# Kernel optimization log

Measured on AMD Instinct MI355X. Metric: run time of the kernel, lower is better.

The kernel has to match this reference:

```python
import jax, jax.numpy as jnp
import numpy as np

B, N, C = 2, 2048, 768
H, HD = 12, 64
HID = 3072
LN_EPS = 1e-5
POL_EPS = 1e-6


def _layer_norm(x, g, b):
    m = jnp.mean(x, axis=-1, keepdims=True)
    v = jnp.mean(jnp.square(x - m), axis=-1, keepdims=True)
    return (x - m) * jax.lax.rsqrt(v + LN_EPS) * g + b


def _softmax_with_policy(attn, policy):
    # attn: [B,H,N,N], policy: [B,N,1]
    n = attn.shape[-1]
    ap = policy.reshape(policy.shape[0], 1, 1, n)  # [B,1,1,N]
    eye = jnp.eye(n, dtype=ap.dtype)[None, None]   # [1,1,N,N]
    ap = ap + (1.0 - ap) * eye                     # always attend to self
    attn = attn - jnp.max(attn, axis=-1, keepdims=True)
    attn = jnp.exp(attn.astype(jnp.float32)) * ap.astype(jnp.float32)
    attn = (attn + POL_EPS / n) / (jnp.sum(attn, axis=-1, keepdims=True) + POL_EPS)
    return attn


def setup_inputs() -> dict:
    key = jax.random.key(0)
    ks = jax.random.split(key, 12)
    s = lambda fan_in: 1.0 / np.sqrt(fan_in)
    x = jax.random.normal(ks[0], (B, N, C), dtype=jnp.float32)
    policy = (jax.random.uniform(ks[1], (B, N, 1)) > 0.5).astype(jnp.float32)
    return {
        "x": x,
        "policy": policy,
        "ln1_g": jnp.ones((C,), jnp.float32),
        "ln1_b": jnp.zeros((C,), jnp.float32),
        "qkv_w": jax.random.uniform(ks[2], (3 * H * HD, C), jnp.float32, -s(C), s(C)),
        "proj_w": jax.random.uniform(ks[3], (C, H * HD), jnp.float32, -s(H * HD), s(H * HD)),
        "proj_b": jnp.zeros((C,), jnp.float32),
        "ln2_g": jnp.ones((C,), jnp.float32),
        "ln2_b": jnp.zeros((C,), jnp.float32),
        "fc1_w": jax.random.uniform(ks[4], (HID, C), jnp.float32, -s(C), s(C)),
        "fc1_b": jnp.zeros((HID,), jnp.float32),
        "fc2_w": jax.random.uniform(ks[5], (C, HID), jnp.float32, -s(HID), s(HID)),
        "fc2_b": jnp.zeros((C,), jnp.float32),
    }


def reference(x, policy, ln1_g, ln1_b, qkv_w, proj_w, proj_b, ln2_g, ln2_b, fc1_w, fc1_b, fc2_w, fc2_b):
    b, n, c = x.shape
    scale = HD ** -0.5
    # --- attention branch (pre-LN) ---
    h = _layer_norm(x, ln1_g, ln1_b)
    qkv = (h @ qkv_w.T).reshape(b, n, 3, H, HD).transpose(2, 0, 3, 1, 4)  # [3,B,H,N,hd]
    q, k, v = qkv[0], qkv[1], qkv[2]
    attn = jnp.einsum("bhqd,bhkd->bhqk", q * scale, k)
    attn = _softmax_with_policy(attn, policy).astype(x.dtype)
    o = jnp.einsum("bhqk,bhkd->bhqd", attn, v).transpose(0, 2, 1, 3).reshape(b, n, H * HD)
    x = x + (o @ proj_w.T + proj_b)  # skip_lam = 1.0, dropout/drop_path = identity
    # --- MLP branch (pre-LN) ---
    h = _layer_norm(x, ln2_g, ln2_b)
    h = jax.nn.gelu(h @ fc1_w.T + fc1_b, approximate=False)  # torch nn.GELU = exact erf
    x = x + (h @ fc2_w.T + fc2_b)
    return x
```

## Files before the change

kernel.cpp:

```cpp
#include <hip/hip_runtime.h>

typedef unsigned short u16;
typedef unsigned int u32;
typedef float f32x4 __attribute__((ext_vector_type(4)));
typedef float f32x16 __attribute__((ext_vector_type(16)));
typedef __bf16 bf16x8 __attribute__((ext_vector_type(8)));
typedef u16 u16x4v __attribute__((ext_vector_type(4)));
typedef u32 u32x2 __attribute__((ext_vector_type(2)));
typedef u32 u32x4 __attribute__((ext_vector_type(4)));

#define NHEAD 12
#define NN 2048
#define CC 768

#define GLOBAL_AS __attribute__((address_space(1)))
#define LDS_AS __attribute__((address_space(3)))

__device__ __forceinline__ u16 tobf(float f) {
  __bf16 h = (__bf16)f;
  return __builtin_bit_cast(u16, h);
}
__device__ __forceinline__ float bf2f(u16 h) {
  u32 u = ((u32)h) << 16;
  return __builtin_bit_cast(float, u);
}
__device__ __forceinline__ void plswap(u32& a, u32& b) {
  asm volatile("v_permlane32_swap_b32 %0, %1" : "+v"(a), "+v"(b));
}
__device__ __forceinline__ void plswapf(float& a, float& b) {
  asm volatile("v_permlane32_swap_b32 %0, %1" : "+v"(a), "+v"(b));
}

#define N4_QKV 442368
#define N4_PROJ 147456
#define N4_FC 589824
__global__ __launch_bounds__(256) void cvt4_kernel(
    const float* __restrict__ a, const float* __restrict__ b,
    const float* __restrict__ c, const float* __restrict__ d,
    u16* __restrict__ oa, u16* __restrict__ ob, u16* __restrict__ oc,
    u16* __restrict__ od) {
  int i = blockIdx.x * 256 + threadIdx.x;
  const float* src;
  u16* dst;
  if (i < N4_QKV) {
    src = a; dst = oa;
  } else if (i < N4_QKV + N4_PROJ) {
    i -= N4_QKV; src = b; dst = ob;
  } else if (i < N4_QKV + N4_PROJ + N4_FC) {
    i -= N4_QKV + N4_PROJ; src = c; dst = oc;
  } else {
    i -= N4_QKV + N4_PROJ + N4_FC; src = d; dst = od;
    if (i >= N4_FC) return;
  }
  float4 v = ((const float4*)src)[i];
  u16x4v o = {tobf(v.x), tobf(v.y), tobf(v.z), tobf(v.w)};
  ((u16x4v*)dst)[i] = o;
}

__global__ __launch_bounds__(256) void ln_kernel(const float* __restrict__ x,
                                                 const float* __restrict__ gw,
                                                 const float* __restrict__ bw,
                                                 u16* __restrict__ out) {
  int row = blockIdx.x * 4 + (threadIdx.x >> 6);
  int lane = threadIdx.x & 63;
  const float* xr = x + (size_t)row * CC + lane * 12;
  float v[12];
  *(float4*)&v[0] = *(const float4*)(xr + 0);
  *(float4*)&v[4] = *(const float4*)(xr + 4);
  *(float4*)&v[8] = *(const float4*)(xr + 8);
  float s = 0.f, sq = 0.f;
#pragma unroll
  for (int j = 0; j < 12; ++j) { s += v[j]; sq += v[j] * v[j]; }
#pragma unroll
  for (int o = 1; o < 64; o <<= 1) { s += __shfl_xor(s, o); sq += __shfl_xor(sq, o); }
  float mean = s * (1.f / CC);
  float var = sq * (1.f / CC) - mean * mean;
  float rs = rsqrtf(var + 1e-5f);
  u16 ob[12];
#pragma unroll
  for (int j = 0; j < 12; ++j) {
    int c = lane * 12 + j;
    ob[j] = tobf((v[j] - mean) * rs * gw[c] + bw[c]);
  }
  u32* orow = (u32*)(out + (size_t)row * CC + lane * 12);
#pragma unroll
  for (int j = 0; j < 6; ++j) orow[j] = (u32)ob[2 * j] | ((u32)ob[2 * j + 1] << 16);
}

template <int BM, int OB, int HASB, int ACT, int RES>
__global__ __launch_bounds__(256) void gemm_kernel(
    const u16* __restrict__ A, const u16* __restrict__ Bw,
    const float* __restrict__ bias, const float* __restrict__ res,
    void* __restrict__ Cout, int M, int N, int K) {
  constexpr int MW = BM / 2;
  constexpr int MF = MW / 16;
  __shared__ __align__(16) u16 Alds[BM * 64];
  __shared__ __align__(16) u16 Blds[128 * 64];
  const int tid = threadIdx.x;
  const int lane = tid & 63, wave = tid >> 6;
  const int l15 = lane & 15, g = lane >> 4;
  const int bm = blockIdx.x * BM, bn = blockIdx.y * 128;
  const int wm = (wave >> 1) * MW, wn = (wave & 1) * 64;
  f32x4 acc[MF][4] = {};

  for (int kt = 0; kt < K; kt += 64) {
#pragma unroll
    for (int i = 0; i < BM / 32; ++i) {
      int ob_ = i * 4096 + wave * 1024;
      int lb = ob_ + lane * 16;
      int row = lb >> 7;
      int cb = (lb & 127) ^ ((row & 7) << 4);
      const u16* sa = A + (size_t)(bm + row) * K + kt + (cb >> 1);
      __builtin_amdgcn_global_load_lds((const GLOBAL_AS void*)sa,
                                       (LDS_AS void*)(Alds + (ob_ >> 1)), 16, 0, 0);
    }
#pragma unroll
    for (int i = 0; i < 4; ++i) {
      int ob_ = i * 4096 + wave * 1024;
      int lb = ob_ + lane * 16;
      int row = lb >> 7;
      int cb = (lb & 127) ^ ((row & 7) << 4);
      const u16* sb = Bw + (size_t)(bn + row) * K + kt + (cb >> 1);
      __builtin_amdgcn_global_load_lds((const GLOBAL_AS void*)sb,
                                       (LDS_AS void*)(Blds + (ob_ >> 1)), 16, 0, 0);
    }
    __syncthreads();
#pragma unroll
    for (int ks = 0; ks < 2; ++ks) {
      bf16x8 af[MF], bfr[4];
#pragma unroll
      for (int mi = 0; mi < MF; ++mi) {
        int row = wm + mi * 16 + l15;
        int cb = (ks * 64 + g * 16) ^ ((row & 7) << 4);
        af[mi] = *(const bf16x8*)&Alds[row * 64 + (cb >> 1)];
      }
#pragma unroll
      for (int ni = 0; ni < 4; ++ni) {
        int row = wn + ni * 16 + l15;
        int cb = (ks * 64 + g * 16) ^ ((row & 7) << 4);
        bfr[ni] = *(const bf16x8*)&Blds[row * 64 + (cb >> 1)];
      }
#pragma unroll
      for (int mi = 0; mi < MF; ++mi)
#pragma unroll
        for (int ni = 0; ni < 4; ++ni)
          acc[mi][ni] = __builtin_amdgcn_mfma_f32_16x16x32_bf16(af[mi], bfr[ni],
                                                                acc[mi][ni], 0, 0, 0);
    }
    __syncthreads();
  }
#pragma unroll
  for (int mi = 0; mi < MF; ++mi) {
#pragma unroll
    for (int ni = 0; ni < 4; ++ni) {
      int col = bn + wn + ni * 16 + l15;
      float bs = HASB ? bias[col] : 0.f;
#pragma unroll
      for (int r = 0; r < 4; ++r) {
        int rowm = bm + wm + mi * 16 + g * 4 + r;
        float v = acc[mi][ni][r] + bs;
        if (ACT) v = 0.5f * v * (1.f + erff(v * 0.70710678118654752f));
        if (RES) v += res[(size_t)rowm * N + col];
        if (OB)
          ((u16*)Cout)[(size_t)rowm * N + col] = tobf(v);
        else
          ((float*)Cout)[(size_t)rowm * N + col] = v;
      }
    }
  }
}

__global__ __launch_bounds__(256) void vsum_kernel(const u16* __restrict__ qkv,
                                                   float* __restrict__ vs) {
  int bh = blockIdx.x, q4 = blockIdx.y;
  int b = bh / NHEAD, h = bh % NHEAD;
  int d = threadIdx.x & 63, part = threadIdx.x >> 6;
  float s = 0.f;
  for (int n = q4 * 512 + part; n < q4 * 512 + 512; n += 4)
    s += bf2f(qkv[(size_t)(b * NN + n) * 2304 + 2 * CC + h * 64 + d]);
  __shared__ float red[256];
  red[threadIdx.x] = s;
  __syncthreads();
  if (threadIdx.x < 64) {
    float t = red[threadIdx.x] + red[threadIdx.x + 64] + red[threadIdx.x + 128] +
              red[threadIdx.x + 192];
    vs[q4 * (24 * 64) + bh * 64 + threadIdx.x] = t;
  }
}

#define SCL2E 0.18033688f
#define TRRD(dst, addr, OFF) \
  asm volatile("ds_read_b64_tr_b16 %0, %1 offset:" OFF : "=v"(dst) : "v"(addr))

__global__ __launch_bounds__(256) void attn32_kernel(const u16* __restrict__ qkv,
                                                     const float* __restrict__ policy,
                                                     float* __restrict__ partO,
                                                     float* __restrict__ partlm) {
  __shared__ __align__(16) u16 Klds[2][4096];
  __shared__ __align__(16) u16 Vlds[2][4096];
  __shared__ u16 PolB[NN];
  __shared__ float alf[4][32];
  const int bh = blockIdx.y, b = bh / NHEAD, h = bh % NHEAD;
  const int qt = blockIdx.x >> 1, half = blockIdx.x & 1;
  const int tid = threadIdx.x, lane = tid & 63, w = tid >> 6;
  const int l31 = lane & 31, hp = lane >> 5, b4 = (lane >> 4) & 1;
  const int q0 = qt * 128 + w * 32;
  const int dv = q0 >> 6;
  const int ktd = (q0 >> 5) & 1;
  const int kv0 = half * 1024;
  const size_t adv = (size_t)64 * 2304;

  bf16x8 qf0, qf1, qf2, qf3;
  {
    const u16* qp = qkv + (size_t)(b * NN + q0 + l31) * 2304 + h * 64 + 8 * hp;
#pragma unroll
    for (int ds = 0; ds < 4; ++ds) {
      bf16x8 r = *(const bf16x8*)(qp + ds * 16);
      bf16x8 o;
#pragma unroll
      for (int j = 0; j < 8; ++j) o[j] = (__bf16)((float)r[j] * SCL2E);
      if (ds == 0) qf0 = o; else if (ds == 1) qf1 = o; else if (ds == 2) qf2 = o; else qf3 = o;
    }
  }

  const u16* ksrc[2];
  const u16* vsrcp[2];
#pragma unroll
  for (int c = 0; c < 2; ++c) {
    int lb = c * 4096 + w * 1024 + lane * 16;
    int row = lb >> 7;
    int cb = (lb & 127) ^ ((row & 7) << 4);
    ksrc[c] = qkv + (size_t)(b * NN + kv0 + row) * 2304 + CC + h * 64 + (cb >> 1);
    int idx0 = (c * 256 + w * 64 + lane) * 8;
    int s0 = idx0 & 15, jj = (idx0 >> 4) & 3, b4v = (idx0 >> 6) & 1,
        pv = (idx0 >> 7) & 1, hv = (idx0 >> 8) & 1, dtv = (idx0 >> 9) & 1,
        mkv = (idx0 >> 10) & 3;
    int key = mkv * 16 + 8 * hv + 4 * pv + jj;
    int d0 = dtv * 32 + 16 * b4v + s0;
    vsrcp[c] = qkv + (size_t)(b * NN + kv0 + key) * 2304 + 2 * CC + h * 64 + d0;
  }
  auto stage = [&](int buf) {
#pragma unroll
    for (int c = 0; c < 2; ++c) {
      __builtin_amdgcn_global_load_lds((const GLOBAL_AS void*)ksrc[c],
                                       (LDS_AS void*)&Klds[buf][c * 2048 + w * 512], 16, 0, 0);
      __builtin_amdgcn_global_load_lds((const GLOBAL_AS void*)vsrcp[c],
                                       (LDS_AS void*)&Vlds[buf][c * 2048 + w * 512], 16, 0, 0);
      ksrc[c] += adv; vsrcp[c] += adv;
    }
  };

  stage(0);
  {
    float4 p0 = *(const float4*)&policy[b * NN + tid * 8];
    float4 p1 = *(const float4*)&policy[b * NN + tid * 8 + 4];
    u16x4v a = {tobf(p0.x), tobf(p0.y), tobf(p0.z), tobf(p0.w)};
    u16x4v c2 = {tobf(p1.x), tobf(p1.y), tobf(p1.z), tobf(p1.w)};
    *(u16x4v*)&PolB[tid * 8] = a;
    *(u16x4v*)&PolB[tid * 8 + 4] = c2;
  }
  __syncthreads();

  float m_cur = -3.0e38f, m_true = -3.0e38f, l_run = 0.f;
  f32x16 accd[2] = {};
  const u32 vbase = (u32)(uintptr_t)(LDS_AS u16*)&Vlds[0][0] +
                    (u32)(2 * (lane & 15) + 128 * b4 + 512 * hp);

  for (int t = 0; t < 16; ++t) {
    const int cur = t & 1;
    const int kvg = kv0 + t * 64;
    if (t < 15) stage(cur ^ 1);

    f32x16 sv0, sv1;
    {
      bf16x8 kf[4];
#pragma unroll
      for (int ds = 0; ds < 4; ++ds) {
        int row = l31;
        int cb = (32 * ds + 16 * hp) ^ ((row & 7) << 4);
        kf[ds] = *(const bf16x8*)((const char*)&Klds[cur][0] + row * 128 + cb);
      }
      f32x16 a = {};
      a = __builtin_amdgcn_mfma_f32_32x32x16_bf16(kf[0], qf0, a, 0, 0, 0);
      a = __builtin_amdgcn_mfma_f32_32x32x16_bf16(kf[1], qf1, a, 0, 0, 0);
      a = __builtin_amdgcn_mfma_f32_32x32x16_bf16(kf[2], qf2, a, 0, 0, 0);
      a = __builtin_amdgcn_mfma_f32_32x32x16_bf16(kf[3], qf3, a, 0, 0, 0);
      sv0 = a;
    }
    {
      bf16x8 kf[4];
#pragma unroll
      for (int ds = 0; ds < 4; ++ds) {
        int row = 32 + l31;
        int cb = (32 * ds + 16 * hp) ^ ((row & 7) << 4);
        kf[ds] = *(const bf16x8*)((const char*)&Klds[cur][0] + row * 128 + cb);
      }
      f32x16 a = {};
      a = __builtin_amdgcn_mfma_f32_32x32x16_bf16(kf[0], qf0, a, 0, 0, 0);
      a = __builtin_amdgcn_mfma_f32_32x32x16_bf16(kf[1], qf1, a, 0, 0, 0);
      a = __builtin_amdgcn_mfma_f32_32x32x16_bf16(kf[2], qf2, a, 0, 0, 0);
      a = __builtin_amdgcn_mfma_f32_32x32x16_bf16(kf[3], qf3, a, 0, 0, 0);
      sv1 = a;
    }

    u32x2 tr[4][2][2];
    {
      u32 vab = vbase + (u32)(cur * 8192);
      TRRD(tr[0][0][0], vab, "0");    TRRD(tr[0][0][1], vab, "256");
      TRRD(tr[0][1][0], vab, "1024"); TRRD(tr[0][1][1], vab, "1280");
      TRRD(tr[1][0][0], vab, "2048"); TRRD(tr[1][0][1], vab, "2304");
      TRRD(tr[1][1][0], vab, "3072"); TRRD(tr[1][1][1], vab, "3328");
      TRRD(tr[2][0][0], vab, "4096"); TRRD(tr[2][0][1], vab, "4352");
      TRRD(tr[3][0][0], vab, "6144"); TRRD(tr[3][0][1], vab, "6400");
      TRRD(tr[2][1][0], vab, "5120"); TRRD(tr[2][1][1], vab, "5376");
      TRRD(tr[3][1][0], vab, "7168"); TRRD(tr[3][1][1], vab, "7424");
    }

    float tmax = sv0[0];
#pragma unroll
    for (int r = 1; r < 16; ++r) tmax = fmaxf(tmax, sv0[r]);
#pragma unroll
    for (int r = 0; r < 16; ++r) tmax = fmaxf(tmax, sv1[r]);
    {
      float t1 = tmax, t2 = tmax;
      plswapf(t1, t2);
      tmax = fmaxf(t1, t2);
    }
    m_true = fmaxf(m_true, tmax);
    const bool defer = __all(tmax <= m_cur + 8.f);
    const float m_new = defer ? m_cur : fmaxf(m_cur, tmax);

    const bool isdiag = ((half * 16 + t) == dv);
    u16 pb[32];
    float psum = 0.f;
#pragma unroll
    for (int kt = 0; kt < 2; ++kt) {
#pragma unroll
      for (int i = 0; i < 4; ++i) {
        u16x4v pq = *(const u16x4v*)&PolB[kvg + kt * 32 + 8 * i + 4 * hp];
#pragma unroll
        for (int rq = 0; rq < 4; ++rq) {
          int r = 4 * i + rq;
          float ap = bf2f(pq[rq]);
          if (isdiag && kt == ktd) ap = ((8 * i + 4 * hp + rq) == l31) ? 1.f : ap;
          float sval = kt ? sv1[r] : sv0[r];
          float e = exp2f(sval - m_new) * ap;
          u16 eb = tobf(e);
          psum += bf2f(eb);
          pb[kt * 16 + r] = eb;
        }
      }
    }
    {
      float s1 = psum, s2 = psum;
      plswapf(s1, s2);
      psum = s1 + s2;
    }
    if (!defer) {
      float alpha = exp2f(m_cur - m_new);
      l_run = l_run * alpha + psum;
      m_cur = m_new;
      if (lane < 32) alf[w][lane] = alpha;
      float4 aq0 = *(const float4*)&alf[w][4 * hp];
      float4 aq1 = *(const float4*)&alf[w][8 + 4 * hp];
      float4 aq2 = *(const float4*)&alf[w][16 + 4 * hp];
      float4 aq3 = *(const float4*)&alf[w][24 + 4 * hp];
#pragma unroll
      for (int dt = 0; dt < 2; ++dt) {
#pragma unroll
        for (int rq = 0; rq < 4; ++rq) {
          accd[dt][0 + rq] *= ((const float*)&aq0)[rq];
          accd[dt][4 + rq] *= ((const float*)&aq1)[rq];
          accd[dt][8 + rq] *= ((const float*)&aq2)[rq];
          accd[dt][12 + rq] *= ((const float*)&aq3)[rq];
        }
      }
    } else {
      l_run += psum;
    }

    u32 PK[4][4];
#pragma unroll
    for (int mk = 0; mk < 4; ++mk) {
      int bs = 16 * (mk >> 1) + 8 * (mk & 1);
      PK[mk][0] = (u32)pb[bs + 0] | ((u32)pb[bs + 1] << 16);
      PK[mk][1] = (u32)pb[bs + 2] | ((u32)pb[bs + 3] << 16);
      PK[mk][2] = (u32)pb[bs + 4] | ((u32)pb[bs + 5] << 16);
      PK[mk][3] = (u32)pb[bs + 6] | ((u32)pb[bs + 7] << 16);
      plswap(PK[mk][2], PK[mk][0]);
      plswap(PK[mk][3], PK[mk][1]);
    }

    asm volatile("s_waitcnt lgkmcnt(0)" ::: "memory");
    __builtin_amdgcn_sched_barrier(0);

#pragma unroll
    for (int mk = 0; mk < 4; ++mk) {
      u32x4 pk4 = {PK[mk][0], PK[mk][1], PK[mk][2], PK[mk][3]};
      bf16x8 pf = __builtin_bit_cast(bf16x8, pk4);
#pragma unroll
      for (int dt = 0; dt < 2; ++dt) {
        u32x4 vv = {tr[mk][dt][0].x, tr[mk][dt][0].y, tr[mk][dt][1].x, tr[mk][dt][1].y};
        bf16x8 vf = __builtin_bit_cast(bf16x8, vv);
        accd[dt] = __builtin_amdgcn_mfma_f32_32x32x16_bf16(pf, vf, accd[dt], 0, 0, 0);
      }
    }
    __syncthreads();
  }

  float sr = exp2f(m_cur - m_true);
  if (lane < 32) {
    alf[w][lane] = sr;
    float2 lm = {l_run * sr, m_true};
    *(float2*)&partlm[2 * ((size_t)(half * 24 + bh) * 2048 + q0 + lane)] = lm;
  }
  float4 sq0 = *(const float4*)&alf[w][4 * hp];
  float4 sq1 = *(const float4*)&alf[w][8 + 4 * hp];
  float4 sq2 = *(const float4*)&alf[w][16 + 4 * hp];
  float4 sq3 = *(const float4*)&alf[w][24 + 4 * hp];
  float* pb2 = partO + ((size_t)(half * 24 + bh) * 2048) * 64;
#pragma unroll
  for (int dt = 0; dt < 2; ++dt) {
#pragma unroll
    for (int i = 0; i < 4; ++i) {
      float4 sqv = (i == 0) ? sq0 : (i == 1) ? sq1 : (i == 2) ? sq2 : sq3;
#pragma unroll
      for (int rq = 0; rq < 4; ++rq) {
        int row = q0 + 8 * i + 4 * hp + rq;
        pb2[(size_t)row * 64 + dt * 32 + l31] = accd[dt][4 * i + rq] * ((const float*)&sqv)[rq];
      }
    }
  }
}

__global__ __launch_bounds__(256) void merge_kernel(const float* __restrict__ partO,
                                                    const float* __restrict__ partlm,
                                                    const float* __restrict__ vs,
                                                    u16* __restrict__ o) {
  int rr = blockIdx.x * 4 + (threadIdx.x >> 6);
  int lane = threadIdx.x & 63;
  int bh = rr >> 11, q = rr & 2047;
  int b = bh / NHEAD, h = bh % NHEAD;
  const float* O1 = partO + ((size_t)bh * 2048 + q) * 64;
  const float* O2 = partO + ((size_t)(24 + bh) * 2048 + q) * 64;
  float2 lm1 = ((const float2*)partlm)[(size_t)bh * 2048 + q];
  float2 lm2 = ((const float2*)partlm)[(size_t)(24 + bh) * 2048 + q];
  float ms = fmaxf(lm1.y, lm2.y);
  float w1 = exp2f(lm1.y - ms), w2 = exp2f(lm2.y - ms);
  float den = lm1.x * w1 + lm2.x * w2 + 1e-6f;
  float vsv = vs[bh * 64 + lane] + vs[1536 + bh * 64 + lane] +
              vs[3072 + bh * 64 + lane] + vs[4608 + bh * 64 + lane];
  float num = O1[lane] * w1 + O2[lane] * w2 + (1e-6f / 2048.f) * vsv;
  o[((size_t)(b * NN + q)) * CC + h * 64 + lane] = tobf(num / den);
}

extern "C" void kernel_launch(void* const* d_in, const int* in_sizes, int n_in,
                              void* d_out, int out_size, void* d_ws, size_t ws_size,
                              hipStream_t stream) {
  const float* x = (const float*)d_in[0];
  const float* policy = (const float*)d_in[1];
  const float* ln1g = (const float*)d_in[2];
  const float* ln1b = (const float*)d_in[3];
  const float* qkvw = (const float*)d_in[4];
  const float* projw = (const float*)d_in[5];
  const float* projb = (const float*)d_in[6];
  const float* ln2g = (const float*)d_in[7];
  const float* ln2b = (const float*)d_in[8];
  const float* fc1w = (const float*)d_in[9];
  const float* fc1b = (const float*)d_in[10];
  const float* fc2w = (const float*)d_in[11];
  const float* fc2b = (const float*)d_in[12];
  float* out = (float*)d_out;

  char* ws = (char*)d_ws;
  size_t off = 0;
  auto alloc = [&](size_t bytes) {
    void* p = ws + off;
    off = (off + bytes + 255) & ~(size_t)255;
    return p;
  };
  u16* wq = (u16*)alloc((size_t)2304 * 768 * 2);
  u16* wp = (u16*)alloc((size_t)768 * 768 * 2);
  u16* w1 = (u16*)alloc((size_t)3072 * 768 * 2);
  u16* w2 = (u16*)alloc((size_t)768 * 3072 * 2);
  u16* hbuf = (u16*)alloc((size_t)4096 * 768 * 2);
  u16* qkv = (u16*)alloc((size_t)4096 * 2304 * 2);
  u16* obuf = (u16*)alloc((size_t)4096 * 768 * 2);
  float* vs = (float*)alloc((size_t)4 * 24 * 64 * 4);
  size_t unionOff = off;
  float* partO = (float*)alloc((size_t)2 * 24 * 2048 * 64 * 4);
  float* partlm = (float*)alloc((size_t)2 * 24 * 2048 * 2 * 4);
  float* x1 = (float*)(ws + unionOff);
  u16* f1 = qkv;

  cvt4_kernel<<<6912, 256, 0, stream>>>(qkvw, projw, fc1w, fc2w, wq, wp, w1, w2);

  ln_kernel<<<1024, 256, 0, stream>>>(x, ln1g, ln1b, hbuf);
  gemm_kernel<128, 1, 0, 0, 0><<<dim3(32, 18), 256, 0, stream>>>(
      hbuf, wq, nullptr, nullptr, qkv, 4096, 2304, 768);
  vsum_kernel<<<dim3(24, 4), 256, 0, stream>>>(qkv, vs);
  attn32_kernel<<<dim3(32, 24), 256, 0, stream>>>(qkv, policy, partO, partlm);
  merge_kernel<<<12288, 256, 0, stream>>>(partO, partlm, vs, obuf);
  gemm_kernel<64, 0, 1, 0, 1><<<dim3(64, 6), 256, 0, stream>>>(
      obuf, wp, projb, x, x1, 4096, 768, 768);
  ln_kernel<<<1024, 256, 0, stream>>>(x1, ln2g, ln2b, hbuf);
  gemm_kernel<128, 1, 1, 1, 0><<<dim3(32, 24), 256, 0, stream>>>(
      hbuf, w1, fc1b, nullptr, f1, 4096, 3072, 768);
  gemm_kernel<64, 0, 1, 0, 1><<<dim3(64, 6), 256, 0, stream>>>(
      f1, w2, fc2b, x1, out, 4096, 768, 3072);
}
```

Baseline: 254.4 us.

## Swizzle GEMM block order and streamline attention softmax arithmetic

The GEMM now remaps its flat block index so that consecutive workgroups are spread across eight groups, with the aim of better L2 locality. The attention kernel keeps the policy in LDS as fp32 instead of bf16 and uses the raw hardware exp2. It converts pairs of probabilities to bf16 with the packed cvt instruction and reduces the row max and row sum as trees instead of serial chains. The KV loop is also forced not to unroll, which limits register pressure and code size. In exchange the policy takes more LDS, and the swizzle assumes the block count divides by eight.

```diff
diff --git a/kernel.cpp b/kernel.cpp
--- a/kernel.cpp
+++ b/kernel.cpp
@@ -23,6 +23,11 @@
 __device__ __forceinline__ float bf2f(u16 h) {
   u32 u = ((u32)h) << 16;
   return __builtin_bit_cast(float, u);
+}
+__device__ __forceinline__ u32 cvtpk(float lo, float hi) {
+  u32 r;
+  asm("v_cvt_pk_bf16_f32 %0, %1, %2" : "=v"(r) : "v"(lo), "v"(hi));
+  return r;
 }
 __device__ __forceinline__ void plswap(u32& a, u32& b) {
   asm volatile("v_permlane32_swap_b32 %0, %1" : "+v"(a), "+v"(b));
@@ -99,7 +104,11 @@
   const int tid = threadIdx.x;
   const int lane = tid & 63, wave = tid >> 6;
   const int l15 = lane & 15, g = lane >> 4;
-  const int bm = blockIdx.x * BM, bn = blockIdx.y * 128;
+  const int nx = gridDim.x;
+  const int flat = blockIdx.y * nx + blockIdx.x;
+  const int cpx = (nx * gridDim.y) >> 3;
+  const int swz = (flat & 7) * cpx + (flat >> 3);
+  const int bm = (swz % nx) * BM, bn = (swz / nx) * 128;
   const int wm = (wave >> 1) * MW, wn = (wave & 1) * 64;
   f32x4 acc[MF][4] = {};
 
@@ -198,7 +207,7 @@
                                                      float* __restrict__ partlm) {
   __shared__ __align__(16) u16 Klds[2][4096];
   __shared__ __align__(16) u16 Vlds[2][4096];
-  __shared__ u16 PolB[NN];
+  __shared__ float PolF[NN];
   __shared__ float alf[4][32];
   const int bh = blockIdx.y, b = bh / NHEAD, h = bh % NHEAD;
   const int qt = blockIdx.x >> 1, half = blockIdx.x & 1;
@@ -254,10 +263,8 @@
   {
     float4 p0 = *(const float4*)&policy[b * NN + tid * 8];
     float4 p1 = *(const float4*)&policy[b * NN + tid * 8 + 4];
-    u16x4v a = {tobf(p0.x), tobf(p0.y), tobf(p0.z), tobf(p0.w)};
-    u16x4v c2 = {tobf(p1.x), tobf(p1.y), tobf(p1.z), tobf(p1.w)};
-    *(u16x4v*)&PolB[tid * 8] = a;
-    *(u16x4v*)&PolB[tid * 8 + 4] = c2;
+    *(float4*)&PolF[tid * 8] = p0;
+    *(float4*)&PolF[tid * 8 + 4] = p1;
   }
   __syncthreads();
 
@@ -266,6 +273,7 @@
   const u32 vbase = (u32)(uintptr_t)(LDS_AS u16*)&Vlds[0][0] +
                     (u32)(2 * (lane & 15) + 128 * b4 + 512 * hp);
 
+#pragma unroll 1
   for (int t = 0; t < 16; ++t) {
     const int cur = t & 1;
     const int kvg = kv0 + t * 64;
@@ -316,11 +324,20 @@
       TRRD(tr[3][1][0], vab, "7168"); TRRD(tr[3][1][1], vab, "7424");
     }
 
-    float tmax = sv0[0];
-#pragma unroll
-    for (int r = 1; r < 16; ++r) tmax = fmaxf(tmax, sv0[r]);
-#pragma unroll
-    for (int r = 0; r < 16; ++r) tmax = fmaxf(tmax, sv1[r]);
+    float ta = fmaxf(fmaxf(sv0[0], sv0[1]), sv0[2]);
+    float tb = fmaxf(fmaxf(sv0[3], sv0[4]), sv0[5]);
+    float tc = fmaxf(fmaxf(sv0[6], sv0[7]), sv0[8]);
+    float td = fmaxf(fmaxf(sv0[9], sv0[10]), sv0[11]);
+    float te = fmaxf(fmaxf(sv0[12], sv0[13]), sv0[14]);
+    float tf = fmaxf(fmaxf(sv0[15], sv1[0]), sv1[1]);
+    float tg = fmaxf(fmaxf(sv1[2], sv1[3]), sv1[4]);
+    float th = fmaxf(fmaxf(sv1[5], sv1[6]), sv1[7]);
+    float ti = fmaxf(fmaxf(sv1[8], sv1[9]), sv1[10]);
+    float tj = fmaxf(fmaxf(sv1[11], sv1[12]), sv1[13]);
+    float tk = fmaxf(sv1[14], sv1[15]);
+    float tmax = fmaxf(fmaxf(fmaxf(fmaxf(ta, tb), fmaxf(tc, td)),
+                             fmaxf(fmaxf(te, tf), fmaxf(tg, th))),
+                       fmaxf(fmaxf(ti, tj), tk));
     {
       float t1 = tmax, t2 = tmax;
       plswapf(t1, t2);
@@ -331,33 +348,42 @@
     const float m_new = defer ? m_cur : fmaxf(m_cur, tmax);
 
     const bool isdiag = ((half * 16 + t) == dv);
-    u16 pb[32];
-    float psum = 0.f;
+    float ev[32];
 #pragma unroll
     for (int kt = 0; kt < 2; ++kt) {
 #pragma unroll
       for (int i = 0; i < 4; ++i) {
-        u16x4v pq = *(const u16x4v*)&PolB[kvg + kt * 32 + 8 * i + 4 * hp];
+        float4 pq = *(const float4*)&PolF[kvg + kt * 32 + 8 * i + 4 * hp];
 #pragma unroll
         for (int rq = 0; rq < 4; ++rq) {
           int r = 4 * i + rq;
-          float ap = bf2f(pq[rq]);
+          float ap = ((const float*)&pq)[rq];
           if (isdiag && kt == ktd) ap = ((8 * i + 4 * hp + rq) == l31) ? 1.f : ap;
           float sval = kt ? sv1[r] : sv0[r];
-          float e = exp2f(sval - m_new) * ap;
-          u16 eb = tobf(e);
-          psum += bf2f(eb);
-          pb[kt * 16 + r] = eb;
+          ev[kt * 16 + r] = __builtin_amdgcn_exp2f(sval - m_new) * ap;
         }
       }
     }
+    u32 wv[16];
+#pragma unroll
+    for (int j = 0; j < 16; ++j) wv[j] = cvtpk(ev[2 * j], ev[2 * j + 1]);
+    float ps[16];
+#pragma unroll
+    for (int j = 0; j < 16; ++j)
+      ps[j] = __builtin_bit_cast(float, wv[j] << 16) +
+              __builtin_bit_cast(float, wv[j] & 0xffff0000u);
+#pragma unroll
+    for (int s = 8; s > 0; s >>= 1)
+#pragma unroll
+      for (int j = 0; j < s; ++j) ps[j] += ps[j + s];
+    float psum = ps[0];
     {
       float s1 = psum, s2 = psum;
       plswapf(s1, s2);
       psum = s1 + s2;
     }
     if (!defer) {
-      float alpha = exp2f(m_cur - m_new);
+      float alpha = __builtin_amdgcn_exp2f(m_cur - m_new);
       l_run = l_run * alpha + psum;
       m_cur = m_new;
       if (lane < 32) alf[w][lane] = alpha;
@@ -382,11 +408,11 @@
     u32 PK[4][4];
 #pragma unroll
     for (int mk = 0; mk < 4; ++mk) {
-      int bs = 16 * (mk >> 1) + 8 * (mk & 1);
-      PK[mk][0] = (u32)pb[bs + 0] | ((u32)pb[bs + 1] << 16);
-      PK[mk][1] = (u32)pb[bs + 2] | ((u32)pb[bs + 3] << 16);
-      PK[mk][2] = (u32)pb[bs + 4] | ((u32)pb[bs + 5] << 16);
-      PK[mk][3] = (u32)pb[bs + 6] | ((u32)pb[bs + 7] << 16);
+      int bw_ = 8 * (mk >> 1) + 4 * (mk & 1);
+      PK[mk][0] = wv[bw_ + 0];
+      PK[mk][1] = wv[bw_ + 1];
+      PK[mk][2] = wv[bw_ + 2];
+      PK[mk][3] = wv[bw_ + 3];
       plswap(PK[mk][2], PK[mk][0]);
       plswap(PK[mk][3], PK[mk][1]);
     }
@@ -408,7 +434,7 @@
     __syncthreads();
   }
 
-  float sr = exp2f(m_cur - m_true);
+  float sr = __builtin_amdgcn_exp2f(m_cur - m_true);
   if (lane < 32) {
     alf[w][lane] = sr;
     float2 lm = {l_run * sr, m_true};
```

Measured after the change: 248.2 us. -2.4%, faster.
